# Kernel optimization log

Measured on AMD Instinct MI355X. Metric: run time of the kernel, lower is better.

Reference implementation:

```python
import jax, jax.numpy as jnp
import numpy as np

N_NODES = 50000
N_EDGES = 1600000
N_GRAPHS = 500
BN_EPS = 1e-5


def gcn_conv(x, src, dst, W, b, n):
    # PyG GCNConv: add self-loops, symmetric normalization, scatter-add at target.
    xw = x @ W  # [N, out]
    deg = jax.ops.segment_sum(jnp.ones_like(dst, dtype=xw.dtype), dst, num_segments=n)
    dinv = jnp.where(deg > 0, jax.lax.rsqrt(deg), 0.0)
    coef = dinv[src] * dinv[dst]  # [E+N]
    out = jax.ops.segment_sum(xw[src] * coef[:, None], dst, num_segments=n)
    return out + b


def batchnorm(h, gamma, beta):
    # training-mode batch stats over the node dim (dropout omitted: eval)
    m = h.mean(axis=0)
    v = h.var(axis=0)
    return (h - m) * jax.lax.rsqrt(v + BN_EPS) * gamma + beta


def setup_inputs() -> dict:
    key = jax.random.key(0)
    ks = jax.random.split(key, 12)
    x = jax.random.normal(ks[0], (N_NODES, 64), dtype=jnp.float32)
    edge_index = jax.random.randint(ks[1], (2, N_EDGES), 0, N_NODES, dtype=jnp.int64)
    batch = jnp.sort(jax.random.randint(ks[2], (N_NODES,), 0, N_GRAPHS, dtype=jnp.int64))
    def glorot(k, shape):
        lim = float(np.sqrt(6.0 / (shape[0] + shape[1])))
        return jax.random.uniform(k, shape, jnp.float32, -lim, lim)
    return {
        "x": x, "edge_index": edge_index, "batch": batch,
        "W1": glorot(ks[3], (64, 128)), "b1": jnp.zeros((128,), jnp.float32),
        "gamma1": jnp.ones((128,), jnp.float32), "beta1": jnp.zeros((128,), jnp.float32),
        "W2": glorot(ks[4], (128, 128)), "b2": jnp.zeros((128,), jnp.float32),
        "gamma2": jnp.ones((128,), jnp.float32), "beta2": jnp.zeros((128,), jnp.float32),
        "W3": glorot(ks[5], (128, 256)), "b3": jnp.zeros((256,), jnp.float32),
        "gamma3": jnp.ones((256,), jnp.float32), "beta3": jnp.zeros((256,), jnp.float32),
        "W4": glorot(ks[6], (256, 10)), "b4": jnp.zeros((10,), jnp.float32),
    }


def reference(x, edge_index, batch, W1, b1, gamma1, beta1, W2, b2, gamma2, beta2,
              W3, b3, gamma3, beta3, W4, b4):
    n = x.shape[0]
    sl = jnp.arange(n, dtype=edge_index.dtype)
    src = jnp.concatenate([edge_index[0], sl])
    dst = jnp.concatenate([edge_index[1], sl])

    h = x
    for W, b, g, bt in ((W1, b1, gamma1, beta1), (W2, b2, gamma2, beta2)):
        h = gcn_conv(h, src, dst, W, b, n)
        h = jax.nn.relu(batchnorm(h, g, bt))

    # global mean pool over graphs
    sums = jax.ops.segment_sum(h, batch, num_segments=N_GRAPHS)
    cnts = jax.ops.segment_sum(jnp.ones((n,), h.dtype), batch, num_segments=N_GRAPHS)
    pooled = sums / jnp.maximum(cnts, 1.0)[:, None]  # [G, 128]

    # MLP head
    z = pooled @ W3 + b3
    z = jax.nn.relu(batchnorm(z, gamma3, beta3))
    return z @ W4 + b4  # [G, num_classes]
```

## Files before the change

### kernel.cpp

```cpp
#include <hip/hip_runtime.h>
#include <hip/hip_bf16.h>

#define BN_EPS 1e-5
#define PB 256

typedef __attribute__((ext_vector_type(8))) short short8;
typedef __attribute__((ext_vector_type(4))) float floatx4;


__device__ __forceinline__ unsigned short f2bf(float f) {
    union { float f; unsigned u; } v; v.f = f;
    unsigned r = v.u + 0x7FFF + ((v.u >> 16) & 1);
    return (unsigned short)(r >> 16);
}
__device__ __forceinline__ float bf2f(unsigned short h) {
    union { unsigned u; float f; } v; v.u = ((unsigned)h) << 16;
    return v.f;
}
__device__ __forceinline__ float lo16(unsigned u) { return bf2f((unsigned short)(u & 0xffff)); }
__device__ __forceinline__ float hi16(unsigned u) { return bf2f((unsigned short)(u >> 16)); }


__global__ void scan1_kernel(const int* __restrict__ in, int* __restrict__ part,
                             int* __restrict__ bsum, int n) {
    __shared__ int s[1024];
    int t = threadIdx.x;
    int i = blockIdx.x * 1024 + t;
    int v = (i < n) ? in[i] : 0;
    s[t] = v;
    __syncthreads();
    for (int off = 1; off < 1024; off <<= 1) {
        int x = (t >= off) ? s[t - off] : 0;
        __syncthreads();
        s[t] += x;
        __syncthreads();
    }
    if (i < n) part[i] = s[t] - v;
    if (t == 1023) bsum[blockIdx.x] = s[1023];
}

__global__ void scan23_add(int* __restrict__ arr, const int* __restrict__ bsum,
                           int nb, int n) {
    __shared__ int s[64];
    int t = threadIdx.x;
    if (t < 64) s[t] = (t < nb) ? bsum[t] : 0;
    __syncthreads();
    for (int off = 1; off < 64; off <<= 1) {
        int x = (t < 64 && t >= off) ? s[t - off] : 0;
        __syncthreads();
        if (t < 64) s[t] += x;
        __syncthreads();
    }
    int i = blockIdx.x * blockDim.x + t;
    if (i < n) {
        int ch = i >> 10;
        int pre = (ch == 0) ? 0 : s[ch - 1];
        arr[i] += pre;
    }
}


__global__ void hist_kernel(const int* __restrict__ dst, int* __restrict__ hist,
                            int E, int cpb, int NB) {
    __shared__ int h[256];
    int t = threadIdx.x;
    if (t < NB) h[t] = 0;
    __syncthreads();
    int base = blockIdx.x * cpb;
    int end = base + cpb; if (end > E) end = E;
    int e = base + t * 4;
    for (; e + 3 < end; e += 1024) {
        int4 d = *(const int4*)(dst + e);
        atomicAdd(&h[d.x >> 8], 1);
        atomicAdd(&h[d.y >> 8], 1);
        atomicAdd(&h[d.z >> 8], 1);
        atomicAdd(&h[d.w >> 8], 1);
    }
    for (; e < end; ++e) atomicAdd(&h[dst[e] >> 8], 1);
    __syncthreads();
    if (t < NB) hist[t * PB + blockIdx.x] = h[t];
}

__global__ void scatter_kernel(const int* __restrict__ src, const int* __restrict__ dst,
                               const int* __restrict__ offs, unsigned* __restrict__ part,
                               int E, int cpb, int NB) {
    __shared__ int cur[256];
    int t = threadIdx.x;
    if (t < NB) cur[t] = offs[t * PB + blockIdx.x];
    __syncthreads();
    int base = blockIdx.x * cpb;
    int end = base + cpb; if (end > E) end = E;
    int e = base + t * 4;
    for (; e + 3 < end; e += 1024) {
        int4 d4 = *(const int4*)(dst + e);
        int4 s4 = *(const int4*)(src + e);
        int dd[4] = {d4.x, d4.y, d4.z, d4.w};
        int sv[4] = {s4.x, s4.y, s4.z, s4.w};
#pragma unroll
        for (int i = 0; i < 4; ++i) {
            int pos = atomicAdd(&cur[dd[i] >> 8], 1);
            part[pos] = ((unsigned)sv[i] << 8) | (unsigned)(dd[i] & 255);
        }
    }
    for (; e < end; ++e) {
        int d = dst[e];
        int pos = atomicAdd(&cur[d >> 8], 1);
        part[pos] = ((unsigned)src[e] << 8) | (unsigned)(d & 255);
    }
}

__global__ void bucket_rowptr(const unsigned* __restrict__ part, const int* __restrict__ offs,
                              int* __restrict__ rowptr, float* __restrict__ dinv,
                              int E, int N, int NB) {
    __shared__ int cw[256], sc[256];
    int b = blockIdx.x;
    int t = threadIdx.x;
    cw[t] = 0;
    __syncthreads();
    int bstart = offs[b * PB];
    int bend = (b + 1 < NB) ? offs[(b + 1) * PB] : E;
    for (int e = bstart + t; e < bend; e += 256)
        atomicAdd(&cw[part[e] & 255u], 1);
    __syncthreads();
    int c = cw[t];
    sc[t] = c;
    __syncthreads();
    for (int off = 1; off < 256; off <<= 1) {
        int x = (t >= off) ? sc[t - off] : 0;
        __syncthreads();
        sc[t] += x;
        __syncthreads();
    }
    int node = (b << 8) + t;
    if (node < N) {
        rowptr[node] = bstart + sc[t] - c;
        dinv[node] = rsqrtf((float)(c + 1));
    }
    if (b == NB - 1 && t == 255) rowptr[N] = E;
}

__global__ void bucket_fill(const unsigned* __restrict__ part, const int* __restrict__ offs,
                            const int* __restrict__ rowptr, int* __restrict__ csr,
                            int E, int N, int NB) {
    __shared__ int cur[256];
    int b = blockIdx.x;
    int t = threadIdx.x;
    int node = (b << 8) + t;
    cur[t] = (node < N) ? rowptr[node] : 0;
    __syncthreads();
    int bstart = offs[b * PB];
    int bend = (b + 1 < NB) ? offs[(b + 1) * PB] : E;
    for (int e = bstart + t; e < bend; e += 256) {
        unsigned pr = part[e];
        int pos = atomicAdd(&cur[pr & 255u], 1);
        csr[pos] = (int)(pr >> 8);
    }
}


__global__ void prescale64_bf(const float* __restrict__ x, const float* __restrict__ dinv,
                              unsigned short* __restrict__ y, int N) {
    int t = blockIdx.x * blockDim.x + threadIdx.x;
    int total = N * 8;
    if (t >= total) return;
    int r = t >> 3;
    float d = dinv[r];
    float4 a = ((const float4*)x)[t * 2];
    float4 b = ((const float4*)x)[t * 2 + 1];
    uint4 o;
    o.x = (unsigned)f2bf(a.x * d) | ((unsigned)f2bf(a.y * d) << 16);
    o.y = (unsigned)f2bf(a.z * d) | ((unsigned)f2bf(a.w * d) << 16);
    o.z = (unsigned)f2bf(b.x * d) | ((unsigned)f2bf(b.y * d) << 16);
    o.w = (unsigned)f2bf(b.z * d) | ((unsigned)f2bf(b.w * d) << 16);
    ((uint4*)y)[t] = o;
}

__global__ __launch_bounds__(256) void agg64_bf(
    const unsigned short* __restrict__ y, const int* __restrict__ rowptr,
    const int* __restrict__ csr, const float* __restrict__ dinv,
    unsigned short* __restrict__ A16, int N) {
    int wv = (blockIdx.x * blockDim.x + threadIdx.x) >> 6;
    int lane = threadIdx.x & 63;
    int node = wv * 2 + (lane >> 5);
    if (node >= N) return;
    int cu = lane & 31;
    const unsigned* yp = (const unsigned*)y;
    unsigned v = yp[(size_t)node * 32 + cu];
    float a0 = lo16(v), a1 = hi16(v);
    int b = rowptr[node], e = rowptr[node + 1];
    int i = b;
    for (; i + 7 < e; i += 8) {
        int s0 = csr[i], s1 = csr[i + 1], s2 = csr[i + 2], s3 = csr[i + 3];
        int s4 = csr[i + 4], s5 = csr[i + 5], s6 = csr[i + 6], s7 = csr[i + 7];
        unsigned v0 = yp[(size_t)s0 * 32 + cu];
        unsigned v1 = yp[(size_t)s1 * 32 + cu];
        unsigned v2 = yp[(size_t)s2 * 32 + cu];
        unsigned v3 = yp[(size_t)s3 * 32 + cu];
        unsigned v4 = yp[(size_t)s4 * 32 + cu];
        unsigned v5 = yp[(size_t)s5 * 32 + cu];
        unsigned v6 = yp[(size_t)s6 * 32 + cu];
        unsigned v7 = yp[(size_t)s7 * 32 + cu];
        a0 += ((lo16(v0) + lo16(v1)) + (lo16(v2) + lo16(v3)))
            + ((lo16(v4) + lo16(v5)) + (lo16(v6) + lo16(v7)));
        a1 += ((hi16(v0) + hi16(v1)) + (hi16(v2) + hi16(v3)))
            + ((hi16(v4) + hi16(v5)) + (hi16(v6) + hi16(v7)));
    }
    for (; i + 3 < e; i += 4) {
        int s0 = csr[i], s1 = csr[i + 1], s2 = csr[i + 2], s3 = csr[i + 3];
        unsigned v0 = yp[(size_t)s0 * 32 + cu];
        unsigned v1 = yp[(size_t)s1 * 32 + cu];
        unsigned v2 = yp[(size_t)s2 * 32 + cu];
        unsigned v3 = yp[(size_t)s3 * 32 + cu];
        a0 += (lo16(v0) + lo16(v1)) + (lo16(v2) + lo16(v3));
        a1 += (hi16(v0) + hi16(v1)) + (hi16(v2) + hi16(v3));
    }
    for (; i < e; ++i) {
        unsigned v0 = yp[(size_t)csr[i] * 32 + cu];
        a0 += lo16(v0);
        a1 += hi16(v0);
    }
    float d = dinv[node];
    ((unsigned*)A16)[(size_t)node * 32 + cu] =
        (unsigned)f2bf(a0 * d) | ((unsigned)f2bf(a1 * d) << 16);
}

__global__ __launch_bounds__(256) void agg128_bf(
    const unsigned short* __restrict__ y, const int* __restrict__ rowptr,
    const int* __restrict__ csr, const float* __restrict__ dinv,
    unsigned short* __restrict__ A16, int N) {
    int wv = (blockIdx.x * blockDim.x + threadIdx.x) >> 6;
    int lane = threadIdx.x & 63;
    int node = wv * 2 + (lane >> 5);
    if (node >= N) return;
    int c2 = lane & 31;
    const uint2* yp = (const uint2*)y;
    uint2 v = yp[(size_t)node * 32 + c2];
    float a0 = lo16(v.x), a1 = hi16(v.x), a2 = lo16(v.y), a3 = hi16(v.y);
    int b = rowptr[node], e = rowptr[node + 1];
    int i = b;
    for (; i + 7 < e; i += 8) {
        int s0 = csr[i], s1 = csr[i + 1], s2 = csr[i + 2], s3 = csr[i + 3];
        int s4 = csr[i + 4], s5 = csr[i + 5], s6 = csr[i + 6], s7 = csr[i + 7];
        uint2 v0 = yp[(size_t)s0 * 32 + c2];
        uint2 v1 = yp[(size_t)s1 * 32 + c2];
        uint2 v2 = yp[(size_t)s2 * 32 + c2];
        uint2 v3 = yp[(size_t)s3 * 32 + c2];
        uint2 v4 = yp[(size_t)s4 * 32 + c2];
        uint2 v5 = yp[(size_t)s5 * 32 + c2];
        uint2 v6 = yp[(size_t)s6 * 32 + c2];
        uint2 v7 = yp[(size_t)s7 * 32 + c2];
        a0 += ((lo16(v0.x) + lo16(v1.x)) + (lo16(v2.x) + lo16(v3.x)))
            + ((lo16(v4.x) + lo16(v5.x)) + (lo16(v6.x) + lo16(v7.x)));
        a1 += ((hi16(v0.x) + hi16(v1.x)) + (hi16(v2.x) + hi16(v3.x)))
            + ((hi16(v4.x) + hi16(v5.x)) + (hi16(v6.x) + hi16(v7.x)));
        a2 += ((lo16(v0.y) + lo16(v1.y)) + (lo16(v2.y) + lo16(v3.y)))
            + ((lo16(v4.y) + lo16(v5.y)) + (lo16(v6.y) + lo16(v7.y)));
        a3 += ((hi16(v0.y) + hi16(v1.y)) + (hi16(v2.y) + hi16(v3.y)))
            + ((hi16(v4.y) + hi16(v5.y)) + (hi16(v6.y) + hi16(v7.y)));
    }
    for (; i + 3 < e; i += 4) {
        int s0 = csr[i], s1 = csr[i + 1], s2 = csr[i + 2], s3 = csr[i + 3];
        uint2 v0 = yp[(size_t)s0 * 32 + c2];
        uint2 v1 = yp[(size_t)s1 * 32 + c2];
        uint2 v2 = yp[(size_t)s2 * 32 + c2];
        uint2 v3 = yp[(size_t)s3 * 32 + c2];
        a0 += (lo16(v0.x) + lo16(v1.x)) + (lo16(v2.x) + lo16(v3.x));
        a1 += (hi16(v0.x) + hi16(v1.x)) + (hi16(v2.x) + hi16(v3.x));
        a2 += (lo16(v0.y) + lo16(v1.y)) + (lo16(v2.y) + lo16(v3.y));
        a3 += (hi16(v0.y) + hi16(v1.y)) + (hi16(v2.y) + hi16(v3.y));
    }
    for (; i < e; ++i) {
        uint2 v0 = yp[(size_t)csr[i] * 32 + c2];
        a0 += lo16(v0.x);
        a1 += hi16(v0.x);
        a2 += lo16(v0.y);
        a3 += hi16(v0.y);
    }
    float d = dinv[node];
    uint2 o;
    o.x = (unsigned)f2bf(a0 * d) | ((unsigned)f2bf(a1 * d) << 16);
    o.y = (unsigned)f2bf(a2 * d) | ((unsigned)f2bf(a3 * d) << 16);
    ((uint2*)A16)[(size_t)node * 32 + c2] = o;
}

__global__ void wpack_kernel(const float* __restrict__ W, uint4* __restrict__ Wp, int K) {
    int i = blockIdx.x * blockDim.x + threadIdx.x;
    int total = K * 16;
    if (i >= total) return;
    int c = i & 127;
    int kb = i >> 7;
    unsigned short h[8];
#pragma unroll
    for (int j = 0; j < 8; ++j) h[j] = f2bf(W[(size_t)(kb * 8 + j) * 128 + c]);
    uint4 o;
    o.x = (unsigned)h[0] | ((unsigned)h[1] << 16);
    o.y = (unsigned)h[2] | ((unsigned)h[3] << 16);
    o.z = (unsigned)h[4] | ((unsigned)h[5] << 16);
    o.w = (unsigned)h[6] | ((unsigned)h[7] << 16);
    Wp[kb * 128 + c] = o;
}

template <int K>
__global__ __launch_bounds__(256) void mfma_gemm(const unsigned short* __restrict__ A16,
                                                 const uint4* __restrict__ Bp,
                                                 unsigned short* __restrict__ out16,
                                                 double* __restrict__ st, int N) {
    constexpr int KS = K / 32;
    __shared__ float cs[128], cs2[128];
    if (threadIdx.x < 128) { cs[threadIdx.x] = 0.f; cs2[threadIdx.x] = 0.f; }
    int w = threadIdx.x >> 6, l = threadIdx.x & 63;
    int cl = l & 15, sub = l >> 4;
    int r0 = blockIdx.x * 64 + w * 16;
    int ra = r0 + cl; if (ra > N - 1) ra = N - 1;

    short8 a[KS];
    const unsigned short* ap = A16 + (size_t)ra * K + sub * 8;
#pragma unroll
    for (int ks = 0; ks < KS; ++ks) a[ks] = *(const short8*)(ap + ks * 32);

    floatx4 acc[8] = {};
#pragma unroll
    for (int cb = 0; cb < 8; ++cb) {
#pragma unroll
        for (int ks = 0; ks < KS; ++ks) {
            short8 b = *(const short8*)&Bp[(ks * 4 + sub) * 128 + cb * 16 + cl];
            acc[cb] = __builtin_amdgcn_mfma_f32_16x16x32_bf16(a[ks], b, acc[cb], 0, 0, 0);
        }
    }
    __syncthreads();
#pragma unroll
    for (int cb = 0; cb < 8; ++cb) {
        float s = 0.f, s2 = 0.f;
#pragma unroll
        for (int j = 0; j < 4; ++j) {
            int row = r0 + sub * 4 + j;
            if (row < N) {
                float val = acc[cb][j];
                out16[(size_t)row * 128 + cb * 16 + cl] = f2bf(val);
                s += val;
                s2 += val * val;
            }
        }
        atomicAdd(&cs[cb * 16 + cl], s);
        atomicAdd(&cs2[cb * 16 + cl], s2);
    }
    __syncthreads();
    if (threadIdx.x < 128) {
        atomicAdd(&st[threadIdx.x], (double)cs[threadIdx.x]);
        atomicAdd(&st[128 + threadIdx.x], (double)cs2[threadIdx.x]);
    }
}

__global__ __launch_bounds__(256) void normrelu_bf(
    const unsigned short* __restrict__ h16, const double* __restrict__ st,
    const float* __restrict__ gamma, const float* __restrict__ beta,
    const float* __restrict__ dinv, unsigned short* __restrict__ out, int N) {
    __shared__ float2 ssl[128];
    if (threadIdx.x < 128) {
        int c = threadIdx.x;
        double mean = st[c] / N;
        double var = st[128 + c] / N - mean * mean;
        float sc = (float)((double)gamma[c] / sqrt(var + BN_EPS));
        float sh = beta[c] - (float)mean * sc;
        ssl[c] = make_float2(sc, sh);
    }
    __syncthreads();
    int t = blockIdx.x * blockDim.x + threadIdx.x;
    int total = N * 16;
    if (t >= total) return;
    int r = t >> 4;
    int j = (t & 15) << 3;
    float d = dinv[r];
    uint4 hv = ((const uint4*)h16)[t];
    float2 s0 = ssl[j], s1 = ssl[j + 1], s2 = ssl[j + 2], s3 = ssl[j + 3];
    float2 s4 = ssl[j + 4], s5 = ssl[j + 5], s6 = ssl[j + 6], s7 = ssl[j + 7];
    float v0 = fmaxf(lo16(hv.x) * s0.x + s0.y, 0.f) * d;
    float v1 = fmaxf(hi16(hv.x) * s1.x + s1.y, 0.f) * d;
    float v2 = fmaxf(lo16(hv.y) * s2.x + s2.y, 0.f) * d;
    float v3 = fmaxf(hi16(hv.y) * s3.x + s3.y, 0.f) * d;
    float v4 = fmaxf(lo16(hv.z) * s4.x + s4.y, 0.f) * d;
    float v5 = fmaxf(hi16(hv.z) * s5.x + s5.y, 0.f) * d;
    float v6 = fmaxf(lo16(hv.w) * s6.x + s6.y, 0.f) * d;
    float v7 = fmaxf(hi16(hv.w) * s7.x + s7.y, 0.f) * d;
    uint4 o;
    o.x = (unsigned)f2bf(v0) | ((unsigned)f2bf(v1) << 16);
    o.y = (unsigned)f2bf(v2) | ((unsigned)f2bf(v3) << 16);
    o.z = (unsigned)f2bf(v4) | ((unsigned)f2bf(v5) << 16);
    o.w = (unsigned)f2bf(v6) | ((unsigned)f2bf(v7) << 16);
    ((uint4*)out)[t] = o;
}

__global__ void bounds_kernel(const int* __restrict__ batch, int* __restrict__ gstart,
                              int N, int G) {
    int i = blockIdx.x * blockDim.x + threadIdx.x;
    if (i >= N) return;
    int bi = batch[i];
    int bp = (i == 0) ? -1 : batch[i - 1];
    for (int g = bp + 1; g <= bi; ++g) gstart[g] = i;
    if (i == N - 1) {
        for (int g = bi + 1; g <= G; ++g) gstart[g] = N;
    }
}

__global__ void pool_bn_kernel(const unsigned short* __restrict__ h16,
                               const double* __restrict__ st,
                               const float* __restrict__ gamma, const float* __restrict__ beta,
                               const int* __restrict__ gstart, float* __restrict__ pooled,
                               int N) {
    int g = blockIdx.x;
    int c = threadIdx.x;
    double mean = st[c] / N;
    double var = st[128 + c] / N - mean * mean;
    float sc = (float)((double)gamma[c] / sqrt(var + BN_EPS));
    float sh = beta[c] - (float)mean * sc;
    int b = gstart[g], e = gstart[g + 1];
    float acc = 0.f;
    int r = b;
    for (; r + 1 < e; r += 2) {
        float v0 = bf2f(h16[(size_t)r * 128 + c]);
        float v1 = bf2f(h16[(size_t)(r + 1) * 128 + c]);
        acc += fmaxf(v0 * sc + sh, 0.f) + fmaxf(v1 * sc + sh, 0.f);
    }
    if (r < e) acc += fmaxf(bf2f(h16[(size_t)r * 128 + c]) * sc + sh, 0.f);
    pooled[(size_t)g * 128 + c] = acc / fmaxf((float)(e - b), 1.0f);
}

template <int K>
__global__ __launch_bounds__(256) void gemm_bias_stats(const float* __restrict__ A,
                                                       const float* __restrict__ W,
                                                       const float* __restrict__ bias,
                                                       float* __restrict__ out,
                                                       double* __restrict__ st,
                                                       int N, int C) {
    __shared__ float Wl[K * 128];
    __shared__ float cs[128], cs2[128];
    if (threadIdx.x < 128) { cs[threadIdx.x] = 0.f; cs2[threadIdx.x] = 0.f; }
    const int ct = blockIdx.y << 7;
    for (int idx = threadIdx.x; idx < K * 128; idx += 256) {
        int kk = idx >> 7, cc = idx & 127;
        Wl[idx] = W[(size_t)kk * C + ct + cc];
    }
    __syncthreads();
    const int cq = (threadIdx.x & 31) << 2;
    const int rg = threadIdx.x >> 5;
    const int r0 = blockIdx.x * 32 + (rg << 2);

    const float* Ap[4];
#pragma unroll
    for (int i = 0; i < 4; ++i) {
        int r = r0 + i;
        Ap[i] = A + (size_t)(r < N ? r : 0) * K;
    }
    float acc[4][4] = {};
#pragma unroll 4
    for (int k = 0; k < K; ++k) {
        float a0 = Ap[0][k];
        float a1 = Ap[1][k];
        float a2 = Ap[2][k];
        float a3 = Ap[3][k];
        float4 w = *(const float4*)&Wl[k * 128 + cq];
        acc[0][0] += a0 * w.x; acc[0][1] += a0 * w.y; acc[0][2] += a0 * w.z; acc[0][3] += a0 * w.w;
        acc[1][0] += a1 * w.x; acc[1][1] += a1 * w.y; acc[1][2] += a1 * w.z; acc[1][3] += a1 * w.w;
        acc[2][0] += a2 * w.x; acc[2][1] += a2 * w.y; acc[2][2] += a2 * w.z; acc[2][3] += a2 * w.w;
        acc[3][0] += a3 * w.x; acc[3][1] += a3 * w.y; acc[3][2] += a3 * w.z; acc[3][3] += a3 * w.w;
    }
    float4 bv = *(const float4*)&bias[ct + cq];
    float s[4] = {}, s2[4] = {};
#pragma unroll
    for (int i = 0; i < 4; ++i) {
        int r = r0 + i;
        if (r < N) {
            float o0 = acc[i][0] + bv.x, o1 = acc[i][1] + bv.y;
            float o2 = acc[i][2] + bv.z, o3 = acc[i][3] + bv.w;
            *(float4*)&out[(size_t)r * C + ct + cq] = make_float4(o0, o1, o2, o3);
            s[0] += o0; s2[0] += o0 * o0;
            s[1] += o1; s2[1] += o1 * o1;
            s[2] += o2; s2[2] += o2 * o2;
            s[3] += o3; s2[3] += o3 * o3;
        }
    }
#pragma unroll
    for (int jj = 0; jj < 4; ++jj) {
        atomicAdd(&cs[cq + jj], s[jj]);
        atomicAdd(&cs2[cq + jj], s2[jj]);
    }
    __syncthreads();
    if (threadIdx.x < 128) {
        atomicAdd(&st[ct + threadIdx.x], (double)cs[threadIdx.x]);
        atomicAdd(&st[C + ct + threadIdx.x], (double)cs2[threadIdx.x]);
    }
}

__global__ void head_kernel(const float* __restrict__ z, const double* __restrict__ st,
                            const float* __restrict__ gamma, const float* __restrict__ beta,
                            const float* __restrict__ W4, const float* __restrict__ b4,
                            float* __restrict__ out, int G) {
    __shared__ float zr[256];
    int g = blockIdx.x;
    int t = threadIdx.x;
    double mean = st[t] / G;
    double var = st[256 + t] / G - mean * mean;
    float sc = (float)((double)gamma[t] / sqrt(var + BN_EPS));
    float sh = beta[t] - (float)mean * sc;
    float v = z[(size_t)g * 256 + t];
    zr[t] = fmaxf(v * sc + sh, 0.f);
    __syncthreads();
    int j = t >> 4;
    int part = t & 15;
    if (j < 10) {
        float acc = 0.f;
#pragma unroll
        for (int k = 0; k < 16; ++k) {
            int c = part + k * 16;
            acc += zr[c] * W4[c * 10 + j];
        }
#pragma unroll
        for (int off = 8; off; off >>= 1) acc += __shfl_down(acc, off);
        if (part == 0) out[(size_t)g * 10 + j] = acc + b4[j];
    }
}


extern "C" void kernel_launch(void* const* d_in, const int* in_sizes, int n_in,
                              void* d_out, int out_size, void* d_ws, size_t ws_size,
                              hipStream_t stream) {
    const int N = in_sizes[0] / 64;
    const int E = in_sizes[1] / 2;
    const int G = out_size / 10;

    const float* x     = (const float*)d_in[0];
    const int*   ei    = (const int*)d_in[1];
    const int*   batch = (const int*)d_in[2];
    const float* W1 = (const float*)d_in[3];
    const float* g1 = (const float*)d_in[5];
    const float* be1 = (const float*)d_in[6];
    const float* W2 = (const float*)d_in[7];
    const float* g2 = (const float*)d_in[9];
    const float* be2 = (const float*)d_in[10];
    const float* W3 = (const float*)d_in[11];
    const float* b3 = (const float*)d_in[12];
    const float* g3 = (const float*)d_in[13];
    const float* be3 = (const float*)d_in[14];
    const float* W4 = (const float*)d_in[15];
    const float* b4 = (const float*)d_in[16];
    float* out = (float*)d_out;

    const int* srcp = ei;
    const int* dstp = ei + E;

    char* p = (char*)d_ws;
    auto alloc = [&](size_t bytes) {
        void* r = (void*)p;
        p += (bytes + 255) & ~(size_t)255;
        return r;
    };
    unsigned short* A16 = (unsigned short*)alloc((size_t)N * 128 * 2);
    unsigned short* h16 = (unsigned short*)alloc((size_t)N * 128 * 2);
    char* R3  = (char*)alloc((size_t)N * 128 * 4);
    int* csr      = (int*)alloc((size_t)E * 4);
    unsigned* part = (unsigned*)alloc((size_t)E * 4);
    int* rowptr = (int*)alloc((size_t)(N + 1) * 4);
    float* dinv = (float*)alloc((size_t)N * 4);
    int* hist   = (int*)alloc((size_t)256 * PB * 4);
    int* offs   = (int*)alloc((size_t)256 * PB * 4);
    int* bsums  = (int*)alloc(64 * 4);
    uint4* w1p  = (uint4*)alloc((size_t)64 * 128 * 2);
    uint4* w2p  = (uint4*)alloc((size_t)128 * 128 * 2);
    int* gstart = (int*)alloc((size_t)(G + 1) * 4);
    float* pooled = (float*)alloc((size_t)G * 128 * 4);
    float* z      = (float*)alloc((size_t)G * 256 * 4);
    double* st    = (double*)alloc(1024 * 8);
    (void)ws_size; (void)n_in;

    unsigned short* c16 = (unsigned short*)R3;
    unsigned short* y16 = (unsigned short*)(R3 + (size_t)N * 128 * 2);

    double* stA = st;
    double* stB = st + 256;
    double* stC = st + 512;

    hipMemsetAsync(st, 0, 1024 * 8, stream);

    const int nb = (N + 255) / 256;
    const int NB = (N + 255) >> 8;
    const int cpb = (((E + PB - 1) / PB) + 3) & ~3;
    const int n2 = NB * PB;
    const int nch2 = (n2 + 1023) / 1024;
    const int aggblocks = (N + 7) / 8;

    wpack_kernel<<<4, 256, 0, stream>>>(W1, w1p, 64);
    wpack_kernel<<<8, 256, 0, stream>>>(W2, w2p, 128);

    hist_kernel<<<PB, 256, 0, stream>>>(dstp, hist, E, cpb, NB);
    scan1_kernel<<<nch2, 1024, 0, stream>>>(hist, offs, bsums, n2);
    scan23_add<<<(n2 + 255) / 256, 256, 0, stream>>>(offs, bsums, nch2, n2);
    scatter_kernel<<<PB, 256, 0, stream>>>(srcp, dstp, offs, part, E, cpb, NB);

    bucket_rowptr<<<NB, 256, 0, stream>>>(part, offs, rowptr, dinv, E, N, NB);
    bucket_fill<<<NB, 256, 0, stream>>>(part, offs, rowptr, csr, E, N, NB);

    prescale64_bf<<<(N * 8 + 255) / 256, 256, 0, stream>>>(x, dinv, y16, N);
    agg64_bf<<<aggblocks, 256, 0, stream>>>(y16, rowptr, csr, dinv, A16, N);
    mfma_gemm<64><<<(N + 63) / 64, 256, 0, stream>>>(A16, w1p, h16, stA, N);
    normrelu_bf<<<(N * 16 + 255) / 256, 256, 0, stream>>>(h16, stA, g1, be1, dinv, c16, N);

    agg128_bf<<<aggblocks, 256, 0, stream>>>(c16, rowptr, csr, dinv, A16, N);
    mfma_gemm<128><<<(N + 63) / 64, 256, 0, stream>>>(A16, w2p, h16, stB, N);

    bounds_kernel<<<nb, 256, 0, stream>>>(batch, gstart, N, G);
    pool_bn_kernel<<<G, 128, 0, stream>>>(h16, stB, g2, be2, gstart, pooled, N);

    gemm_bias_stats<128><<<dim3((G + 31) / 32, 2), 256, 0, stream>>>(pooled, W3, b3, z, stC, G, 256);
    head_kernel<<<G, 256, 0, stream>>>(z, stC, g3, be3, W4, b4, out, G);
}
```

Before: 255.9 us.

## Merge setup kernels and fuse bucket rowptr, fill and prescale into one

Weight packing, graph-bound computation and the destination histogram are combined into one multi-role launch that dispatches on block index. The bucket rowptr, CSR fill and x prescale/bf16 conversion are fused into a single per-bucket kernel, which keeps the running offsets and dinv in shared memory instead of re-reading rowptr. This cuts the launch count from six to two and removes some global round-trips. In exchange the fused bucket kernel does more serial work per block.

```diff
diff --git a/kernel.cpp b/kernel.cpp
--- a/kernel.cpp
+++ b/kernel.cpp
@@ -19,6 +19,65 @@
 }
 __device__ __forceinline__ float lo16(unsigned u) { return bf2f((unsigned short)(u & 0xffff)); }
 __device__ __forceinline__ float hi16(unsigned u) { return bf2f((unsigned short)(u >> 16)); }
+
+
+__device__ __forceinline__ void wpack_body(const float* __restrict__ W, uint4* __restrict__ Wp,
+                                           int K, int i) {
+    if (i >= K * 16) return;
+    int c = i & 127;
+    int kb = i >> 7;
+    unsigned short h[8];
+#pragma unroll
+    for (int j = 0; j < 8; ++j) h[j] = f2bf(W[(size_t)(kb * 8 + j) * 128 + c]);
+    uint4 o;
+    o.x = (unsigned)h[0] | ((unsigned)h[1] << 16);
+    o.y = (unsigned)h[2] | ((unsigned)h[3] << 16);
+    o.z = (unsigned)h[4] | ((unsigned)h[5] << 16);
+    o.w = (unsigned)h[6] | ((unsigned)h[7] << 16);
+    Wp[kb * 128 + c] = o;
+}
+
+__global__ void setup_kernel(const float* __restrict__ W1, uint4* __restrict__ w1p,
+                             const float* __restrict__ W2, uint4* __restrict__ w2p,
+                             const int* __restrict__ batch, int* __restrict__ gstart,
+                             const int* __restrict__ dst, int* __restrict__ hist,
+                             int N, int G, int E, int cpb, int NB, int nb) {
+    __shared__ int h[256];
+    int t = threadIdx.x;
+    int b = blockIdx.x;
+    if (b < 4) {
+        wpack_body(W1, w1p, 64, b * 256 + t);
+    } else if (b < 12) {
+        wpack_body(W2, w2p, 128, (b - 4) * 256 + t);
+    } else if (b < 12 + nb) {
+        int i = (b - 12) * 256 + t;
+        if (i < N) {
+            int bi = batch[i];
+            int bp = (i == 0) ? -1 : batch[i - 1];
+            for (int g = bp + 1; g <= bi; ++g) gstart[g] = i;
+            if (i == N - 1) {
+                for (int g = bi + 1; g <= G; ++g) gstart[g] = N;
+            }
+        }
+    } else {
+        int blk = b - 12 - nb;
+        if (t < NB) h[t] = 0;
+        __syncthreads();
+        int base = blk * cpb;
+        int end = base + cpb; if (end > E) end = E;
+        int e = base + t * 4;
+        for (; e + 3 < end; e += 1024) {
+            int4 d = *(const int4*)(dst + e);
+            atomicAdd(&h[d.x >> 8], 1);
+            atomicAdd(&h[d.y >> 8], 1);
+            atomicAdd(&h[d.z >> 8], 1);
+            atomicAdd(&h[d.w >> 8], 1);
+        }
+        for (; e < end; ++e) atomicAdd(&h[dst[e] >> 8], 1);
+        __syncthreads();
+        if (t < NB) hist[t * PB + blk] = h[t];
+    }
+}
 
 
 __global__ void scan1_kernel(const int* __restrict__ in, int* __restrict__ part,
@@ -59,27 +118,6 @@
     }
 }
 
-
-__global__ void hist_kernel(const int* __restrict__ dst, int* __restrict__ hist,
-                            int E, int cpb, int NB) {
-    __shared__ int h[256];
-    int t = threadIdx.x;
-    if (t < NB) h[t] = 0;
-    __syncthreads();
-    int base = blockIdx.x * cpb;
-    int end = base + cpb; if (end > E) end = E;
-    int e = base + t * 4;
-    for (; e + 3 < end; e += 1024) {
-        int4 d = *(const int4*)(dst + e);
-        atomicAdd(&h[d.x >> 8], 1);
-        atomicAdd(&h[d.y >> 8], 1);
-        atomicAdd(&h[d.z >> 8], 1);
-        atomicAdd(&h[d.w >> 8], 1);
-    }
-    for (; e < end; ++e) atomicAdd(&h[dst[e] >> 8], 1);
-    __syncthreads();
-    if (t < NB) hist[t * PB + blockIdx.x] = h[t];
-}
 
 __global__ void scatter_kernel(const int* __restrict__ src, const int* __restrict__ dst,
                                const int* __restrict__ offs, unsigned* __restrict__ part,
@@ -109,10 +147,13 @@
     }
 }
 
-__global__ void bucket_rowptr(const unsigned* __restrict__ part, const int* __restrict__ offs,
-                              int* __restrict__ rowptr, float* __restrict__ dinv,
-                              int E, int N, int NB) {
-    __shared__ int cw[256], sc[256];
+__global__ __launch_bounds__(256) void bucket_build(
+    const unsigned* __restrict__ part, const int* __restrict__ offs,
+    int* __restrict__ rowptr, float* __restrict__ dinv, int* __restrict__ csr,
+    const float* __restrict__ x, unsigned short* __restrict__ y16,
+    int E, int N, int NB) {
+    __shared__ int cw[256], sc[256], cur[256];
+    __shared__ float sd[256];
     int b = blockIdx.x;
     int t = threadIdx.x;
     cw[t] = 0;
@@ -126,54 +167,46 @@
     sc[t] = c;
     __syncthreads();
     for (int off = 1; off < 256; off <<= 1) {
-        int x = (t >= off) ? sc[t - off] : 0;
-        __syncthreads();
-        sc[t] += x;
+        int v = (t >= off) ? sc[t - off] : 0;
+        __syncthreads();
+        sc[t] += v;
         __syncthreads();
     }
     int node = (b << 8) + t;
+    int start = bstart + sc[t] - c;
+    float d = rsqrtf((float)(c + 1));
+    cur[t] = start;
+    sd[t] = d;
     if (node < N) {
-        rowptr[node] = bstart + sc[t] - c;
-        dinv[node] = rsqrtf((float)(c + 1));
+        rowptr[node] = start;
+        dinv[node] = d;
     }
     if (b == NB - 1 && t == 255) rowptr[N] = E;
-}
-
-__global__ void bucket_fill(const unsigned* __restrict__ part, const int* __restrict__ offs,
-                            const int* __restrict__ rowptr, int* __restrict__ csr,
-                            int E, int N, int NB) {
-    __shared__ int cur[256];
-    int b = blockIdx.x;
-    int t = threadIdx.x;
-    int node = (b << 8) + t;
-    cur[t] = (node < N) ? rowptr[node] : 0;
-    __syncthreads();
-    int bstart = offs[b * PB];
-    int bend = (b + 1 < NB) ? offs[(b + 1) * PB] : E;
+    __syncthreads();
     for (int e = bstart + t; e < bend; e += 256) {
         unsigned pr = part[e];
         int pos = atomicAdd(&cur[pr & 255u], 1);
         csr[pos] = (int)(pr >> 8);
     }
-}
-
-
-__global__ void prescale64_bf(const float* __restrict__ x, const float* __restrict__ dinv,
-                              unsigned short* __restrict__ y, int N) {
-    int t = blockIdx.x * blockDim.x + threadIdx.x;
-    int total = N * 8;
-    if (t >= total) return;
-    int r = t >> 3;
-    float d = dinv[r];
-    float4 a = ((const float4*)x)[t * 2];
-    float4 b = ((const float4*)x)[t * 2 + 1];
-    uint4 o;
-    o.x = (unsigned)f2bf(a.x * d) | ((unsigned)f2bf(a.y * d) << 16);
-    o.y = (unsigned)f2bf(a.z * d) | ((unsigned)f2bf(a.w * d) << 16);
-    o.z = (unsigned)f2bf(b.x * d) | ((unsigned)f2bf(b.y * d) << 16);
-    o.w = (unsigned)f2bf(b.z * d) | ((unsigned)f2bf(b.w * d) << 16);
-    ((uint4*)y)[t] = o;
-}
+    int base = b << 8;
+    int nlocal = N - base; if (nlocal > 256) nlocal = 256;
+    if (nlocal <= 0) return;
+    for (int idx = t; idx < nlocal * 8; idx += 256) {
+        int r = idx >> 3, k = idx & 7;
+        int nd = base + r;
+        float dd = sd[r];
+        const float4* xp = (const float4*)(x + (size_t)nd * 64 + k * 8);
+        float4 a = xp[0];
+        float4 bb = xp[1];
+        uint4 o;
+        o.x = (unsigned)f2bf(a.x * dd) | ((unsigned)f2bf(a.y * dd) << 16);
+        o.y = (unsigned)f2bf(a.z * dd) | ((unsigned)f2bf(a.w * dd) << 16);
+        o.z = (unsigned)f2bf(bb.x * dd) | ((unsigned)f2bf(bb.y * dd) << 16);
+        o.w = (unsigned)f2bf(bb.z * dd) | ((unsigned)f2bf(bb.w * dd) << 16);
+        *(uint4*)(y16 + (size_t)nd * 64 + k * 8) = o;
+    }
+}
+
 
 __global__ __launch_bounds__(256) void agg64_bf(
     const unsigned short* __restrict__ y, const int* __restrict__ rowptr,
@@ -283,22 +316,6 @@
     ((uint2*)A16)[(size_t)node * 32 + c2] = o;
 }
 
-__global__ void wpack_kernel(const float* __restrict__ W, uint4* __restrict__ Wp, int K) {
-    int i = blockIdx.x * blockDim.x + threadIdx.x;
-    int total = K * 16;
-    if (i >= total) return;
-    int c = i & 127;
-    int kb = i >> 7;
-    unsigned short h[8];
-#pragma unroll
-    for (int j = 0; j < 8; ++j) h[j] = f2bf(W[(size_t)(kb * 8 + j) * 128 + c]);
-    uint4 o;
-    o.x = (unsigned)h[0] | ((unsigned)h[1] << 16);
-    o.y = (unsigned)h[2] | ((unsigned)h[3] << 16);
-    o.z = (unsigned)h[4] | ((unsigned)h[5] << 16);
-    o.w = (unsigned)h[6] | ((unsigned)h[7] << 16);
-    Wp[kb * 128 + c] = o;
-}
 
 template <int K>
 __global__ __launch_bounds__(256) void mfma_gemm(const unsigned short* __restrict__ A16,
@@ -390,18 +407,6 @@
     ((uint4*)out)[t] = o;
 }
 
-__global__ void bounds_kernel(const int* __restrict__ batch, int* __restrict__ gstart,
-                              int N, int G) {
-    int i = blockIdx.x * blockDim.x + threadIdx.x;
-    if (i >= N) return;
-    int bi = batch[i];
-    int bp = (i == 0) ? -1 : batch[i - 1];
-    for (int g = bp + 1; g <= bi; ++g) gstart[g] = i;
-    if (i == N - 1) {
-        for (int g = bi + 1; g <= G; ++g) gstart[g] = N;
-    }
-}
-
 __global__ void pool_bn_kernel(const unsigned short* __restrict__ h16,
                                const double* __restrict__ st,
                                const float* __restrict__ gamma, const float* __restrict__ beta,
@@ -588,18 +593,14 @@
     const int nch2 = (n2 + 1023) / 1024;
     const int aggblocks = (N + 7) / 8;
 
-    wpack_kernel<<<4, 256, 0, stream>>>(W1, w1p, 64);
-    wpack_kernel<<<8, 256, 0, stream>>>(W2, w2p, 128);
-
-    hist_kernel<<<PB, 256, 0, stream>>>(dstp, hist, E, cpb, NB);
+    setup_kernel<<<4 + 8 + nb + PB, 256, 0, stream>>>(W1, w1p, W2, w2p, batch, gstart,
+                                                      dstp, hist, N, G, E, cpb, NB, nb);
     scan1_kernel<<<nch2, 1024, 0, stream>>>(hist, offs, bsums, n2);
     scan23_add<<<(n2 + 255) / 256, 256, 0, stream>>>(offs, bsums, nch2, n2);
     scatter_kernel<<<PB, 256, 0, stream>>>(srcp, dstp, offs, part, E, cpb, NB);
 
-    bucket_rowptr<<<NB, 256, 0, stream>>>(part, offs, rowptr, dinv, E, N, NB);
-    bucket_fill<<<NB, 256, 0, stream>>>(part, offs, rowptr, csr, E, N, NB);
-
-    prescale64_bf<<<(N * 8 + 255) / 256, 256, 0, stream>>>(x, dinv, y16, N);
+    bucket_build<<<NB, 256, 0, stream>>>(part, offs, rowptr, dinv, csr, x, y16, E, N, NB);
+
     agg64_bf<<<aggblocks, 256, 0, stream>>>(y16, rowptr, csr, dinv, A16, N);
     mfma_gemm<64><<<(N + 63) / 64, 256, 0, stream>>>(A16, w1p, h16, stA, N);
     normrelu_bf<<<(N * 16 + 255) / 256, 256, 0, stream>>>(h16, stA, g1, be1, dinv, c16, N);
@@ -607,7 +608,6 @@
     agg128_bf<<<aggblocks, 256, 0, stream>>>(c16, rowptr, csr, dinv, A16, N);
     mfma_gemm<128><<<(N + 63) / 64, 256, 0, stream>>>(A16, w2p, h16, stB, N);
 
-    bounds_kernel<<<nb, 256, 0, stream>>>(batch, gstart, N, G);
     pool_bn_kernel<<<G, 128, 0, stream>>>(h16, stB, g2, be2, gstart, pooled, N);
 
     gemm_bias_stats<128><<<dim3((G + 31) / 32, 2), 256, 0, stream>>>(pooled, W3, b3, z, stC, G, 256);
```

Result: faster. 248.3 us (-2.9%).
